# Optimization experiments

Hardware: AMD Instinct MI355X
Metric: run time of the kernel (lower is better)

The kernel has to match this reference:

```python
import jax, jax.numpy as jnp
import numpy as np

N = 100000        # points
C_IN = 64         # in_planes
C_OUT = 64        # out_planes (== mid_planes)
SHARE = 8         # share_planes
NS = 16           # nsample
CW = C_OUT // SHARE  # attention channels (8)
EPS = 1e-5


def _bn(x, gamma, beta):
    # PointBatchNorm in training mode: normalize over all axes except channel (last)
    ax = tuple(range(x.ndim - 1))
    m = jnp.mean(x, axis=ax)
    v = jnp.var(x, axis=ax)
    return gamma * (x - m) * jax.lax.rsqrt(v + EPS) + beta


def setup_inputs() -> dict:
    key = jax.random.key(0)
    ks = jax.random.split(key, 20)
    s = 0.05
    inp = {
        "p": jax.random.normal(ks[0], (N, 3), jnp.float32) * 5.0,
        "x": jax.random.normal(ks[1], (N, C_IN), jnp.float32),
        "o": jnp.array([N], jnp.int32),
        "idx": jax.random.randint(ks[2], (N, NS), 0, N, jnp.int32),
        # q/k/v linears
        "Wq": jax.random.normal(ks[3], (C_IN, C_OUT), jnp.float32) * s,
        "bq": jnp.zeros((C_OUT,), jnp.float32),
        "Wk": jax.random.normal(ks[4], (C_IN, C_OUT), jnp.float32) * s,
        "bk": jnp.zeros((C_OUT,), jnp.float32),
        "Wv": jax.random.normal(ks[5], (C_IN, C_OUT), jnp.float32) * s,
        "bv": jnp.zeros((C_OUT,), jnp.float32),
        # linear_p: Linear(3,3) -> BN(3) -> ReLU -> Linear(3,out)
        "Wp1": jax.random.normal(ks[6], (3, 3), jnp.float32) * 0.5,
        "bp1": jnp.zeros((3,), jnp.float32),
        "gp": jnp.ones((3,), jnp.float32),
        "betap": jnp.zeros((3,), jnp.float32),
        "Wp2": jax.random.normal(ks[7], (3, C_OUT), jnp.float32) * s,
        "bp2": jnp.zeros((C_OUT,), jnp.float32),
        # linear_w: BN(mid)->ReLU->Linear(mid, CW)->BN(CW)->ReLU->Linear(CW, CW)
        "gw1": jnp.ones((C_OUT,), jnp.float32),
        "bw1": jnp.zeros((C_OUT,), jnp.float32),
        "Ww1": jax.random.normal(ks[8], (C_OUT, CW), jnp.float32) * s,
        "bww1": jnp.zeros((CW,), jnp.float32),
        "gw2": jnp.ones((CW,), jnp.float32),
        "bw2": jnp.zeros((CW,), jnp.float32),
        "Ww2": jax.random.normal(ks[9], (CW, CW), jnp.float32) * s,
        "bww2": jnp.zeros((CW,), jnp.float32),
    }
    return inp


def reference(p, x, o, idx,
              Wq, bq, Wk, bk, Wv, bv,
              Wp1, bp1, gp, betap, Wp2, bp2,
              gw1, bw1, Ww1, bww1, gw2, bw2, Ww2, bww2):
    relu = jax.nn.relu
    x_q = x @ Wq + bq                       # [n, mid]
    x_k = x @ Wk + bk                       # [n, mid]
    x_v = x @ Wv + bv                       # [n, out]
    # knn_query_and_group: gather neighbors (idx precomputed), with relative xyz
    p_r0 = p[idx] - p[:, None, :]           # [n, ns, 3]
    xk_g = x_k[idx]                         # [n, ns, mid]
    xv_g = x_v[idx]                         # [n, ns, out]
    # linear_p
    p_r = relu(_bn(p_r0 @ Wp1 + bp1, gp, betap)) @ Wp2 + bp2   # [n, ns, out]
    # einops.reduce 'n ns (i j) -> n ns j' with j=mid_planes: i==1 -> identity
    r_qk = xk_g - x_q[:, None, :] + p_r     # [n, ns, mid]
    # linear_w
    w = relu(_bn(r_qk, gw1, bw1)) @ Ww1 + bww1          # [n, ns, CW]
    w = relu(_bn(w, gw2, bw2)) @ Ww2 + bww2             # [n, ns, CW]
    w = jax.nn.softmax(w, axis=1)                        # softmax over neighbors
    # shared-channel weighted sum
    v = (xv_g + p_r).reshape(N, NS, SHARE, CW)           # [n, ns, s, i]
    out = jnp.einsum('ntsi,nti->nsi', v, w)              # [n, s, i]
    return out.reshape(N, C_OUT)
```

## Files before the change

kernel.cpp:

```cpp
#include <hip/hip_runtime.h>
#include <math.h>

#define NPTS 100000
#define NSAMP 16
#define NROWS (NPTS*NSAMP)
#define EPS 1e-5f

#define NQKV ((NPTS + 63)/64)
#define GRID_B 1024
#define GRID_C 2048
#define GRID_D 2048
#define GRID_E 2048

#define S_BN1A 0
#define S_BN1B 4
#define S_BN2A 8
#define S_BN2B 72
#define S_BN3A 136
#define S_BN3B 144
#define S_PARTB 160
#define S_PARTC (S_PARTB + GRID_B*8)
#define S_PARTD (S_PARTC + GRID_C*128)

typedef __attribute__((ext_vector_type(8))) short bf16x8;
typedef __attribute__((ext_vector_type(4))) float f32x4;

__device__ __forceinline__ unsigned short f2bf(float f) {
    unsigned int x = __float_as_uint(f);
    unsigned int r = (x + 0x7fffu + ((x >> 16) & 1u)) >> 16;
    return (unsigned short)r;
}
__device__ __forceinline__ float bf2f(unsigned short u) {
    return __uint_as_float(((unsigned int)u) << 16);
}
__device__ __forceinline__ float rlF(float v, int t) {
    return __int_as_float(__builtin_amdgcn_readlane(__float_as_int(v), t));
}

__global__ __launch_bounds__(256) void qkv_bn1_kernel(
    const float* __restrict__ x,
    const float* __restrict__ Wq, const float* __restrict__ bq,
    const float* __restrict__ Wk, const float* __restrict__ bk,
    const float* __restrict__ Wv, const float* __restrict__ bv,
    float* __restrict__ xq, unsigned short* __restrict__ xkb,
    unsigned short* __restrict__ xvb,
    const float* __restrict__ p, const int* __restrict__ idx,
    const float* __restrict__ Wp1, const float* __restrict__ bp1,
    float* __restrict__ part)
{
    __shared__ __align__(16) float xsh[64][68];
    __shared__ __align__(16) float wsh[64][64];
    __shared__ float red16[4][6];
    const int tid = threadIdx.x;

    if (blockIdx.x >= NQKV) {
        const int b = blockIdx.x - NQKV;
        float w9[9], bb[3];
        #pragma unroll
        for (int i = 0; i < 9; ++i) w9[i] = Wp1[i];
        #pragma unroll
        for (int i = 0; i < 3; ++i) bb[i] = bp1[i];

        float s0=0.f,s1=0.f,s2=0.f,q0=0.f,q1=0.f,q2=0.f;
        for (int row = b*256 + tid; row < NROWS; row += GRID_B*256) {
            const int n = row >> 4;
            const int j = idx[row];
            const float d0 = p[j*3+0] - p[n*3+0];
            const float d1 = p[j*3+1] - p[n*3+1];
            const float d2 = p[j*3+2] - p[n*3+2];
            const float t0 = d0*w9[0] + d1*w9[3] + d2*w9[6] + bb[0];
            const float t1 = d0*w9[1] + d1*w9[4] + d2*w9[7] + bb[1];
            const float t2 = d0*w9[2] + d1*w9[5] + d2*w9[8] + bb[2];
            s0 += t0; s1 += t1; s2 += t2;
            q0 += t0*t0; q1 += t1*t1; q2 += t2*t2;
        }
        #pragma unroll
        for (int m = 32; m >= 1; m >>= 1) {
            s0 += __shfl_xor(s0, m); s1 += __shfl_xor(s1, m); s2 += __shfl_xor(s2, m);
            q0 += __shfl_xor(q0, m); q1 += __shfl_xor(q1, m); q2 += __shfl_xor(q2, m);
        }
        const int lane = tid & 63, wid = tid >> 6;
        if (lane == 0) {
            red16[wid][0]=s0; red16[wid][1]=s1; red16[wid][2]=s2;
            red16[wid][3]=q0; red16[wid][4]=q1; red16[wid][5]=q2;
        }
        __syncthreads();
        if (tid < 6)
            part[b*8 + tid] = red16[0][tid]+red16[1][tid]+red16[2][tid]+red16[3][tid];
        return;
    }

    const int r0 = blockIdx.x * 64;
    {
        const int row = tid >> 4, c4 = tid & 15;
        #pragma unroll
        for (int rr = 0; rr < 4; ++rr) {
            const int r = row + rr*16;
            const int gr = r0 + r;
            float4 v = (gr < NPTS) ? *(const float4*)&x[(size_t)gr*64 + c4*4]
                                   : make_float4(0.f, 0.f, 0.f, 0.f);
            *(float4*)&xsh[r][c4*4] = v;
        }
    }

    const int tr = tid >> 4, tc = tid & 15;

    for (int m = 0; m < 3; ++m) {
        const float* __restrict__ W  = (m == 0) ? Wq : (m == 1) ? Wk : Wv;
        const float* __restrict__ bs = (m == 0) ? bq : (m == 1) ? bk : bv;

        __syncthreads();
        for (int l = tid; l < 1024; l += 256)
            *(float4*)&wsh[l >> 4][(l & 15)*4] = *(const float4*)&W[l*4];
        __syncthreads();

        float acc[4][4];
        {
            const float4 b4 = *(const float4*)&bs[tc*4];
            #pragma unroll
            for (int rr = 0; rr < 4; ++rr) {
                acc[rr][0] = b4.x; acc[rr][1] = b4.y;
                acc[rr][2] = b4.z; acc[rr][3] = b4.w;
            }
        }

        #pragma unroll 4
        for (int k4 = 0; k4 < 16; ++k4) {
            float4 xr[4];
            #pragma unroll
            for (int rr = 0; rr < 4; ++rr)
                xr[rr] = *(const float4*)&xsh[tr + 16*rr][k4*4];
            float4 wr[4];
            #pragma unroll
            for (int kk = 0; kk < 4; ++kk)
                wr[kk] = *(const float4*)&wsh[k4*4 + kk][tc*4];
            #pragma unroll
            for (int rr = 0; rr < 4; ++rr) {
                acc[rr][0] += xr[rr].x*wr[0].x + xr[rr].y*wr[1].x + xr[rr].z*wr[2].x + xr[rr].w*wr[3].x;
                acc[rr][1] += xr[rr].x*wr[0].y + xr[rr].y*wr[1].y + xr[rr].z*wr[2].y + xr[rr].w*wr[3].y;
                acc[rr][2] += xr[rr].x*wr[0].z + xr[rr].y*wr[1].z + xr[rr].z*wr[2].z + xr[rr].w*wr[3].z;
                acc[rr][3] += xr[rr].x*wr[0].w + xr[rr].y*wr[1].w + xr[rr].z*wr[2].w + xr[rr].w*wr[3].w;
            }
        }

        #pragma unroll
        for (int rr = 0; rr < 4; ++rr) {
            const int gr = r0 + tr + 16*rr;
            if (gr < NPTS) {
                if (m == 0) {
                    float4 o;
                    o.x = acc[rr][0]; o.y = acc[rr][1]; o.z = acc[rr][2]; o.w = acc[rr][3];
                    *(float4*)&xq[(size_t)gr*64 + tc*4] = o;
                } else {
                    unsigned short* dst = (m == 1) ? xkb : xvb;
                    ushort4 o;
                    o.x = f2bf(acc[rr][0]); o.y = f2bf(acc[rr][1]);
                    o.z = f2bf(acc[rr][2]); o.w = f2bf(acc[rr][3]);
                    *(ushort4*)&dst[(size_t)gr*64 + tc*4] = o;
                }
            }
        }
    }
}

__global__ __launch_bounds__(256) void bn_fin_kernel(
    const float* __restrict__ part, int nblk, int stride, int nch,
    const float* __restrict__ g, const float* __restrict__ beta,
    float* __restrict__ aout, float* __restrict__ bout)
{
    const int c = blockIdx.x;
    const int tid = threadIdx.x;
    float s = 0.f, q = 0.f;
    for (int b = tid; b < nblk; b += 256) {
        s += part[(size_t)b*stride + c];
        q += part[(size_t)b*stride + nch + c];
    }
    #pragma unroll
    for (int m = 32; m >= 1; m >>= 1) { s += __shfl_xor(s, m); q += __shfl_xor(q, m); }
    __shared__ float rs[4], rq[4];
    if ((tid & 63) == 0) { rs[tid >> 6] = s; rq[tid >> 6] = q; }
    __syncthreads();
    if (tid == 0) {
        s = rs[0]+rs[1]+rs[2]+rs[3];
        q = rq[0]+rq[1]+rq[2]+rq[3];
        const float inv = 1.0f / (float)NROWS;
        const float mean = s * inv;
        const float var = fmaxf(q * inv - mean*mean, 0.f);
        const float a = g[c] * rsqrtf(var + EPS);
        aout[c] = a;
        bout[c] = beta[c] - a * mean;
    }
}

__global__ __launch_bounds__(256, 8) void bn2_stats_kernel(
    const float* __restrict__ p, const int* __restrict__ idx,
    const float* __restrict__ xq, const unsigned short* __restrict__ xkb,
    const float* __restrict__ Wp1, const float* __restrict__ bp1,
    const float* __restrict__ Wp2, const float* __restrict__ bp2,
    const float* __restrict__ st, float* __restrict__ part)
{
    const int tid = threadIdx.x, lane = tid & 63, wid = tid >> 6;
    float w9[9], bb[3], a1[3], b1[3];
    #pragma unroll
    for (int i = 0; i < 9; ++i) w9[i] = Wp1[i];
    #pragma unroll
    for (int i = 0; i < 3; ++i) { bb[i] = bp1[i]; a1[i] = st[S_BN1A+i]; b1[i] = st[S_BN1B+i]; }
    const float wc0 = Wp2[lane], wc1 = Wp2[64+lane], wc2 = Wp2[128+lane], bpc = bp2[lane];
    const int lane16 = lane & 15;

    float s = 0.f, q = 0.f;
    const int nw = gridDim.x * 4;
    for (int pt = blockIdx.x*4 + wid; pt < NPTS; pt += nw) {
        const float xqc = xq[(size_t)pt*64 + lane];
        const int jreg = idx[pt*16 + lane16];
        const float pn0 = p[pt*3], pn1 = p[pt*3+1], pn2 = p[pt*3+2];
        const float d0 = p[jreg*3] - pn0, d1 = p[jreg*3+1] - pn1, d2 = p[jreg*3+2] - pn2;
        const float t0 = d0*w9[0] + d1*w9[3] + d2*w9[6] + bb[0];
        const float t1 = d0*w9[1] + d1*w9[4] + d2*w9[7] + bb[1];
        const float t2 = d0*w9[2] + d1*w9[5] + d2*w9[8] + bb[2];
        const float h0 = fmaxf(a1[0]*t0 + b1[0], 0.f);
        const float h1 = fmaxf(a1[1]*t1 + b1[1], 0.f);
        const float h2 = fmaxf(a1[2]*t2 + b1[2], 0.f);

        #pragma unroll
        for (int t = 0; t < 16; ++t) {
            const int jt = __builtin_amdgcn_readlane(jreg, t);
            const float g0 = rlF(h0, t), g1 = rlF(h1, t), g2 = rlF(h2, t);
            const float pr = fmaf(g0, wc0, fmaf(g1, wc1, fmaf(g2, wc2, bpc)));
            const float r = bf2f(xkb[(size_t)jt*64 + lane]) - xqc + pr;
            s += r; q = fmaf(r, r, q);
        }
    }
    __shared__ float redS[4][64], redQ[4][64];
    redS[wid][lane] = s; redQ[wid][lane] = q;
    __syncthreads();
    if (tid < 64) {
        const float S = redS[0][tid]+redS[1][tid]+redS[2][tid]+redS[3][tid];
        const float Q = redQ[0][tid]+redQ[1][tid]+redQ[2][tid]+redQ[3][tid];
        part[(size_t)blockIdx.x*128 + tid] = S;
        part[(size_t)blockIdx.x*128 + 64 + tid] = Q;
    }
}

__global__ __launch_bounds__(256, 8) void w1_kernel(
    const float* __restrict__ p, const int* __restrict__ idx,
    const float* __restrict__ xq, const unsigned short* __restrict__ xkb,
    const float* __restrict__ Wp1, const float* __restrict__ bp1,
    const float* __restrict__ Wp2, const float* __restrict__ bp2,
    const float* __restrict__ Ww1, const float* __restrict__ bww1,
    const float* __restrict__ st, unsigned short* __restrict__ w1out,
    float* __restrict__ part)
{
    __shared__ unsigned short hl[4][16][64];
    const int tid = threadIdx.x, lane = tid & 63, wid = tid >> 6;

    float w9[9], bb[3], a1[3], b1[3];
    #pragma unroll
    for (int i = 0; i < 9; ++i) w9[i] = Wp1[i];
    #pragma unroll
    for (int i = 0; i < 3; ++i) { bb[i] = bp1[i]; a1[i] = st[S_BN1A+i]; b1[i] = st[S_BN1B+i]; }

    const int c = lane;
    const float wc0 = Wp2[c], wc1 = Wp2[64+c], wc2 = Wp2[128+c], bpc = bp2[c];
    const float a2c = st[S_BN2A + c], b2c = st[S_BN2B + c];
    const int lane16 = lane & 15;
    const int kgrp = lane >> 4;

    bf16x8 aF0, aF1;
    {
        const int m = lane16;
        #pragma unroll
        for (int i = 0; i < 8; ++i) {
            const int k0 = kgrp*4 + (i & 3) + 16*(i >> 2);
            const int i0 = (m < 8) ? (k0*8 + m) : 0;
            const int i1 = (m < 8) ? ((k0 + 32)*8 + m) : 0;
            aF0[i] = (m < 8) ? (short)f2bf(Ww1[i0]) : (short)0;
            aF1[i] = (m < 8) ? (short)f2bf(Ww1[i1]) : (short)0;
        }
    }
    f32x4 cb;
    #pragma unroll
    for (int r = 0; r < 4; ++r) cb[r] = bww1[(kgrp*4 + r) & 7];

    float s3[4] = {0.f,0.f,0.f,0.f}, q3[4] = {0.f,0.f,0.f,0.f};
    const int nw = gridDim.x * 4;
    for (int pt = blockIdx.x*4 + wid; pt < NPTS; pt += nw) {
        const float xqc = xq[(size_t)pt*64 + lane];
        const int jreg = idx[pt*16 + lane16];
        const float pn0 = p[pt*3], pn1 = p[pt*3+1], pn2 = p[pt*3+2];
        const float d0 = p[jreg*3] - pn0, d1 = p[jreg*3+1] - pn1, d2 = p[jreg*3+2] - pn2;
        const float t0v = d0*w9[0] + d1*w9[3] + d2*w9[6] + bb[0];
        const float t1v = d0*w9[1] + d1*w9[4] + d2*w9[7] + bb[1];
        const float t2v = d0*w9[2] + d1*w9[5] + d2*w9[8] + bb[2];
        const float h0 = fmaxf(a1[0]*t0v + b1[0], 0.f);
        const float h1 = fmaxf(a1[1]*t1v + b1[1], 0.f);
        const float h2 = fmaxf(a1[2]*t2v + b1[2], 0.f);

        #pragma unroll
        for (int t = 0; t < 16; ++t) {
            const int jt = __builtin_amdgcn_readlane(jreg, t);
            const float g0 = rlF(h0, t), g1 = rlF(h1, t), g2 = rlF(h2, t);
            const float pr = fmaf(g0, wc0, fmaf(g1, wc1, fmaf(g2, wc2, bpc)));
            const float r = bf2f(xkb[(size_t)jt*64 + lane]) - xqc + pr;
            const float hv = fmaxf(fmaf(a2c, r, b2c), 0.f);
            hl[wid][t][lane ^ ((t & 7) << 3)] = f2bf(hv);
        }

        const int t = lane16;
        const int key = (t & 7) << 3;
        union { bf16x8 v; uint2 u[2]; } b0u, b1u;
        b0u.u[0] = *(const uint2*)&hl[wid][t][(kgrp*4)      ^ key];
        b0u.u[1] = *(const uint2*)&hl[wid][t][(kgrp*4 + 16) ^ key];
        b1u.u[0] = *(const uint2*)&hl[wid][t][(kgrp*4 + 32) ^ key];
        b1u.u[1] = *(const uint2*)&hl[wid][t][(kgrp*4 + 48) ^ key];

        f32x4 acc = __builtin_amdgcn_mfma_f32_16x16x32_bf16(aF0, b0u.v, cb, 0, 0, 0);
        acc = __builtin_amdgcn_mfma_f32_16x16x32_bf16(aF1, b1u.v, acc, 0, 0, 0);

        if (lane < 32) {
            ushort4 o;
            o.x = f2bf(acc[0]); o.y = f2bf(acc[1]);
            o.z = f2bf(acc[2]); o.w = f2bf(acc[3]);
            *(ushort4*)&w1out[(size_t)pt*128 + lane16*8 + kgrp*4] = o;
            #pragma unroll
            for (int r = 0; r < 4; ++r) {
                s3[r] += acc[r];
                q3[r] = fmaf(acc[r], acc[r], q3[r]);
            }
        }
    }

    #pragma unroll
    for (int m = 8; m >= 1; m >>= 1) {
        #pragma unroll
        for (int r = 0; r < 4; ++r) {
            s3[r] += __shfl_xor(s3[r], m);
            q3[r] += __shfl_xor(q3[r], m);
        }
    }
    __shared__ float redS[4][8], redQ[4][8];
    if (lane == 0 || lane == 16) {
        const int jb = (lane >> 4) * 4;
        #pragma unroll
        for (int r = 0; r < 4; ++r) { redS[wid][jb+r] = s3[r]; redQ[wid][jb+r] = q3[r]; }
    }
    __syncthreads();
    if (tid < 8) {
        const float S = redS[0][tid]+redS[1][tid]+redS[2][tid]+redS[3][tid];
        const float Q = redQ[0][tid]+redQ[1][tid]+redQ[2][tid]+redQ[3][tid];
        part[(size_t)blockIdx.x*16 + tid]     = S;
        part[(size_t)blockIdx.x*16 + 8 + tid] = Q;
    }
}

__global__ __launch_bounds__(256, 8) void out_kernel(
    const float* __restrict__ p, const int* __restrict__ idx,
    const unsigned short* __restrict__ xvb, const unsigned short* __restrict__ w1b,
    const float* __restrict__ Wp1, const float* __restrict__ bp1,
    const float* __restrict__ Wp2, const float* __restrict__ bp2,
    const float* __restrict__ Ww2, const float* __restrict__ bww2,
    const float* __restrict__ st, float* __restrict__ out)
{
    __shared__ float wl[4][16][8];
    const int tid = threadIdx.x, lane = tid & 63, wid = tid >> 6;
    const int j8 = lane & 7, t0 = lane >> 3;
    const int lane16 = lane & 15;

    float w9[9], bb[3], a1[3], b1[3];
    #pragma unroll
    for (int i = 0; i < 9; ++i) w9[i] = Wp1[i];
    #pragma unroll
    for (int i = 0; i < 3; ++i) { bb[i] = bp1[i]; a1[i] = st[S_BN1A+i]; b1[i] = st[S_BN1B+i]; }
    float ww2c[8];
    #pragma unroll
    for (int i = 0; i < 8; ++i) ww2c[i] = Ww2[i*8 + j8];
    const float a3j = st[S_BN3A + j8], b3j = st[S_BN3B + j8];
    const float bw2j = bww2[j8];
    const int c = lane;
    const float wc0 = Wp2[c], wc1 = Wp2[64+c], wc2 = Wp2[128+c], bpc = bp2[c];

    const int nw = gridDim.x * 4;
    for (int pt = blockIdx.x*4 + wid; pt < NPTS; pt += nw) {
        const int jreg = idx[pt*16 + lane16];
        const float pn0 = p[pt*3], pn1 = p[pt*3+1], pn2 = p[pt*3+2];
        const float d0 = p[jreg*3] - pn0, d1 = p[jreg*3+1] - pn1, d2 = p[jreg*3+2] - pn2;
        const float t1v = d0*w9[0] + d1*w9[3] + d2*w9[6] + bb[0];
        const float t2v = d0*w9[1] + d1*w9[4] + d2*w9[7] + bb[1];
        const float t3v = d0*w9[2] + d1*w9[5] + d2*w9[8] + bb[2];
        const float h0 = fmaxf(a1[0]*t1v + b1[0], 0.f);
        const float h1 = fmaxf(a1[1]*t2v + b1[1], 0.f);
        const float h2 = fmaxf(a1[2]*t3v + b1[2], 0.f);

        const float val0 = bf2f(w1b[(size_t)pt*128 + lane]);
        const float val1 = bf2f(w1b[(size_t)pt*128 + 64 + lane]);
        const float r0 = fmaxf(a3j*val0 + b3j, 0.f);
        const float r1 = fmaxf(a3j*val1 + b3j, 0.f);
        float v0 = bw2j, v1 = bw2j;
        const int gbase = lane & 56;
        #pragma unroll
        for (int jj = 0; jj < 8; ++jj) {
            v0 += __shfl(r0, gbase + jj) * ww2c[jj];
            v1 += __shfl(r1, gbase + jj) * ww2c[jj];
        }

        float m = fmaxf(v0, v1);
        m = fmaxf(m, __shfl_xor(m, 8));
        m = fmaxf(m, __shfl_xor(m, 16));
        m = fmaxf(m, __shfl_xor(m, 32));
        float e0 = __expf(v0 - m), e1 = __expf(v1 - m);
        float ssum = e0 + e1;
        ssum += __shfl_xor(ssum, 8);
        ssum += __shfl_xor(ssum, 16);
        ssum += __shfl_xor(ssum, 32);
        const float inv = 1.0f / ssum;
        wl[wid][t0][j8]     = e0 * inv;
        wl[wid][t0 + 8][j8] = e1 * inv;

        float acc = 0.f;
        #pragma unroll
        for (int t = 0; t < 16; ++t) {
            const int jt = __builtin_amdgcn_readlane(jreg, t);
            const float g0 = rlF(h0, t), g1 = rlF(h1, t), g2 = rlF(h2, t);
            const float pr = fmaf(g0, wc0, fmaf(g1, wc1, fmaf(g2, wc2, bpc)));
            const float wt = wl[wid][t][j8];
            acc = fmaf(bf2f(xvb[(size_t)jt*64 + c]) + pr, wt, acc);
        }
        out[(size_t)pt*64 + c] = acc;
    }
}

extern "C" void kernel_launch(void* const* d_in, const int* in_sizes, int n_in,
                              void* d_out, int out_size, void* d_ws, size_t ws_size,
                              hipStream_t stream)
{
    const float* p    = (const float*)d_in[0];
    const float* x    = (const float*)d_in[1];
    const int*   idx  = (const int*)d_in[3];
    const float* Wq   = (const float*)d_in[4];
    const float* bq   = (const float*)d_in[5];
    const float* Wk   = (const float*)d_in[6];
    const float* bk   = (const float*)d_in[7];
    const float* Wv   = (const float*)d_in[8];
    const float* bv   = (const float*)d_in[9];
    const float* Wp1  = (const float*)d_in[10];
    const float* bp1  = (const float*)d_in[11];
    const float* gp   = (const float*)d_in[12];
    const float* betap= (const float*)d_in[13];
    const float* Wp2  = (const float*)d_in[14];
    const float* bp2  = (const float*)d_in[15];
    const float* gw1  = (const float*)d_in[16];
    const float* bw1  = (const float*)d_in[17];
    const float* Ww1  = (const float*)d_in[18];
    const float* bww1 = (const float*)d_in[19];
    const float* gw2  = (const float*)d_in[20];
    const float* bw2  = (const float*)d_in[21];
    const float* Ww2  = (const float*)d_in[22];
    const float* bww2 = (const float*)d_in[23];

    float* out = (float*)d_out;
    float* ws  = (float*)d_ws;

    float*          xq  = ws;
    unsigned short* xkb = (unsigned short*)(ws + (size_t)NPTS*64);
    unsigned short* xvb = (unsigned short*)(ws + (size_t)NPTS*96);
    unsigned short* w1b = (unsigned short*)(ws + (size_t)NPTS*128);
    float*          st  = ws + (size_t)NPTS*192;

    qkv_bn1_kernel<<<NQKV + GRID_B, 256, 0, stream>>>(
        x, Wq, bq, Wk, bk, Wv, bv, xq, xkb, xvb,
        p, idx, Wp1, bp1, st + S_PARTB);
    bn_fin_kernel<<<3, 256, 0, stream>>>(st + S_PARTB, GRID_B, 8, 3, gp, betap,
                                         st + S_BN1A, st + S_BN1B);

    bn2_stats_kernel<<<GRID_C, 256, 0, stream>>>(p, idx, xq, xkb, Wp1, bp1, Wp2, bp2,
                                                 st, st + S_PARTC);
    bn_fin_kernel<<<64, 256, 0, stream>>>(st + S_PARTC, GRID_C, 128, 64, gw1, bw1,
                                          st + S_BN2A, st + S_BN2B);

    w1_kernel<<<GRID_D, 256, 0, stream>>>(p, idx, xq, xkb, Wp1, bp1, Wp2, bp2,
                                          Ww1, bww1, st, w1b, st + S_PARTD);
    bn_fin_kernel<<<8, 256, 0, stream>>>(st + S_PARTD, GRID_D, 16, 8, gw2, bw2,
                                         st + S_BN3A, st + S_BN3B);

    out_kernel<<<GRID_E, 256, 0, stream>>>(p, idx, xvb, w1b, Wp1, bp1, Wp2, bp2,
                                           Ww2, bww2, st, out);
}
```

Before: 251.5 us.

## Store xq in bf16, prefetch next point's gathers, switch MFMA to f16, drop softmax max

Several changes land together. xq is now stored as bf16 like xk and xv, which halves its write and read traffic. The three gather kernels prefetch the next point's idx, position and xq or w1 values before working on the current one, so load latency overlaps with compute. The w1 MFMA now uses f16 inputs instead of bf16, bf16 packing uses the hardware v_cvt_pk_bf16_f32 instruction, and the softmax drops its max-subtraction shuffles. In exchange, precision drops for xq, and removing the max makes the softmax able to overflow if logits are large.

```diff
diff --git a/kernel.cpp b/kernel.cpp
--- a/kernel.cpp
+++ b/kernel.cpp
@@ -22,16 +22,16 @@
 #define S_PARTC (S_PARTB + GRID_B*8)
 #define S_PARTD (S_PARTC + GRID_C*128)
 
-typedef __attribute__((ext_vector_type(8))) short bf16x8;
+typedef __attribute__((ext_vector_type(8))) _Float16 f16x8;
 typedef __attribute__((ext_vector_type(4))) float f32x4;
 
-__device__ __forceinline__ unsigned short f2bf(float f) {
-    unsigned int x = __float_as_uint(f);
-    unsigned int r = (x + 0x7fffu + ((x >> 16) & 1u)) >> 16;
-    return (unsigned short)r;
-}
 __device__ __forceinline__ float bf2f(unsigned short u) {
     return __uint_as_float(((unsigned int)u) << 16);
+}
+__device__ __forceinline__ unsigned int cvt_pk_bf16(float lo, float hi) {
+    unsigned int r;
+    asm("v_cvt_pk_bf16_f32 %0, %1, %2" : "=v"(r) : "v"(lo), "v"(hi));
+    return r;
 }
 __device__ __forceinline__ float rlF(float v, int t) {
     return __int_as_float(__builtin_amdgcn_readlane(__float_as_int(v), t));
@@ -42,7 +42,7 @@
     const float* __restrict__ Wq, const float* __restrict__ bq,
     const float* __restrict__ Wk, const float* __restrict__ bk,
     const float* __restrict__ Wv, const float* __restrict__ bv,
-    float* __restrict__ xq, unsigned short* __restrict__ xkb,
+    unsigned short* __restrict__ xqb, unsigned short* __restrict__ xkb,
     unsigned short* __restrict__ xvb,
     const float* __restrict__ p, const int* __restrict__ idx,
     const float* __restrict__ Wp1, const float* __restrict__ bp1,
@@ -108,6 +108,7 @@
     for (int m = 0; m < 3; ++m) {
         const float* __restrict__ W  = (m == 0) ? Wq : (m == 1) ? Wk : Wv;
         const float* __restrict__ bs = (m == 0) ? bq : (m == 1) ? bk : bv;
+        unsigned short* __restrict__ dst = (m == 0) ? xqb : (m == 1) ? xkb : xvb;
 
         __syncthreads();
         for (int l = tid; l < 1024; l += 256)
@@ -147,17 +148,10 @@
         for (int rr = 0; rr < 4; ++rr) {
             const int gr = r0 + tr + 16*rr;
             if (gr < NPTS) {
-                if (m == 0) {
-                    float4 o;
-                    o.x = acc[rr][0]; o.y = acc[rr][1]; o.z = acc[rr][2]; o.w = acc[rr][3];
-                    *(float4*)&xq[(size_t)gr*64 + tc*4] = o;
-                } else {
-                    unsigned short* dst = (m == 1) ? xkb : xvb;
-                    ushort4 o;
-                    o.x = f2bf(acc[rr][0]); o.y = f2bf(acc[rr][1]);
-                    o.z = f2bf(acc[rr][2]); o.w = f2bf(acc[rr][3]);
-                    *(ushort4*)&dst[(size_t)gr*64 + tc*4] = o;
-                }
+                uint2 o;
+                o.x = cvt_pk_bf16(acc[rr][0], acc[rr][1]);
+                o.y = cvt_pk_bf16(acc[rr][2], acc[rr][3]);
+                *(uint2*)&dst[(size_t)gr*64 + tc*4] = o;
             }
         }
     }
@@ -194,7 +188,7 @@
 
 __global__ __launch_bounds__(256, 8) void bn2_stats_kernel(
     const float* __restrict__ p, const int* __restrict__ idx,
-    const float* __restrict__ xq, const unsigned short* __restrict__ xkb,
+    const unsigned short* __restrict__ xqb, const unsigned short* __restrict__ xkb,
     const float* __restrict__ Wp1, const float* __restrict__ bp1,
     const float* __restrict__ Wp2, const float* __restrict__ bp2,
     const float* __restrict__ st, float* __restrict__ part)
@@ -207,14 +201,29 @@
     for (int i = 0; i < 3; ++i) { bb[i] = bp1[i]; a1[i] = st[S_BN1A+i]; b1[i] = st[S_BN1B+i]; }
     const float wc0 = Wp2[lane], wc1 = Wp2[64+lane], wc2 = Wp2[128+lane], bpc = bp2[lane];
     const int lane16 = lane & 15;
+    const int nw = gridDim.x * 4;
 
     float s = 0.f, q = 0.f;
-    const int nw = gridDim.x * 4;
-    for (int pt = blockIdx.x*4 + wid; pt < NPTS; pt += nw) {
-        const float xqc = xq[(size_t)pt*64 + lane];
-        const int jreg = idx[pt*16 + lane16];
-        const float pn0 = p[pt*3], pn1 = p[pt*3+1], pn2 = p[pt*3+2];
-        const float d0 = p[jreg*3] - pn0, d1 = p[jreg*3+1] - pn1, d2 = p[jreg*3+2] - pn2;
+    int pt = blockIdx.x*4 + wid;
+    int jn = 0; float xqn = 0.f, pn0 = 0.f, pn1 = 0.f, pn2 = 0.f;
+    float pj0 = 0.f, pj1 = 0.f, pj2 = 0.f;
+    if (pt < NPTS) {
+        jn = idx[pt*16 + lane16];
+        xqn = bf2f(xqb[(size_t)pt*64 + lane]);
+        pn0 = p[pt*3]; pn1 = p[pt*3+1]; pn2 = p[pt*3+2];
+        pj0 = p[jn*3]; pj1 = p[jn*3+1]; pj2 = p[jn*3+2];
+    }
+    while (pt < NPTS) {
+        const int jreg = jn;
+        const float xqc = xqn;
+        const float d0 = pj0 - pn0, d1 = pj1 - pn1, d2 = pj2 - pn2;
+        const int ptn = pt + nw;
+        if (ptn < NPTS) {
+            jn = idx[ptn*16 + lane16];
+            xqn = bf2f(xqb[(size_t)ptn*64 + lane]);
+            pn0 = p[ptn*3]; pn1 = p[ptn*3+1]; pn2 = p[ptn*3+2];
+            pj0 = p[jn*3]; pj1 = p[jn*3+1]; pj2 = p[jn*3+2];
+        }
         const float t0 = d0*w9[0] + d1*w9[3] + d2*w9[6] + bb[0];
         const float t1 = d0*w9[1] + d1*w9[4] + d2*w9[7] + bb[1];
         const float t2 = d0*w9[2] + d1*w9[5] + d2*w9[8] + bb[2];
@@ -230,6 +239,7 @@
             const float r = bf2f(xkb[(size_t)jt*64 + lane]) - xqc + pr;
             s += r; q = fmaf(r, r, q);
         }
+        pt = ptn;
     }
     __shared__ float redS[4][64], redQ[4][64];
     redS[wid][lane] = s; redQ[wid][lane] = q;
@@ -244,14 +254,14 @@
 
 __global__ __launch_bounds__(256, 8) void w1_kernel(
     const float* __restrict__ p, const int* __restrict__ idx,
-    const float* __restrict__ xq, const unsigned short* __restrict__ xkb,
+    const unsigned short* __restrict__ xqb, const unsigned short* __restrict__ xkb,
     const float* __restrict__ Wp1, const float* __restrict__ bp1,
     const float* __restrict__ Wp2, const float* __restrict__ bp2,
     const float* __restrict__ Ww1, const float* __restrict__ bww1,
     const float* __restrict__ st, unsigned short* __restrict__ w1out,
     float* __restrict__ part)
 {
-    __shared__ unsigned short hl[4][16][64];
+    __shared__ __align__(16) _Float16 hl[4][16][64];
     const int tid = threadIdx.x, lane = tid & 63, wid = tid >> 6;
 
     float w9[9], bb[3], a1[3], b1[3];
@@ -266,7 +276,7 @@
     const int lane16 = lane & 15;
     const int kgrp = lane >> 4;
 
-    bf16x8 aF0, aF1;
+    f16x8 aF0, aF1;
     {
         const int m = lane16;
         #pragma unroll
@@ -274,8 +284,8 @@
             const int k0 = kgrp*4 + (i & 3) + 16*(i >> 2);
             const int i0 = (m < 8) ? (k0*8 + m) : 0;
             const int i1 = (m < 8) ? ((k0 + 32)*8 + m) : 0;
-            aF0[i] = (m < 8) ? (short)f2bf(Ww1[i0]) : (short)0;
-            aF1[i] = (m < 8) ? (short)f2bf(Ww1[i1]) : (short)0;
+            aF0[i] = (m < 8) ? (_Float16)Ww1[i0] : (_Float16)0.f;
+            aF1[i] = (m < 8) ? (_Float16)Ww1[i1] : (_Float16)0.f;
         }
     }
     f32x4 cb;
@@ -284,11 +294,26 @@
 
     float s3[4] = {0.f,0.f,0.f,0.f}, q3[4] = {0.f,0.f,0.f,0.f};
     const int nw = gridDim.x * 4;
-    for (int pt = blockIdx.x*4 + wid; pt < NPTS; pt += nw) {
-        const float xqc = xq[(size_t)pt*64 + lane];
-        const int jreg = idx[pt*16 + lane16];
-        const float pn0 = p[pt*3], pn1 = p[pt*3+1], pn2 = p[pt*3+2];
-        const float d0 = p[jreg*3] - pn0, d1 = p[jreg*3+1] - pn1, d2 = p[jreg*3+2] - pn2;
+    int pt = blockIdx.x*4 + wid;
+    int jn = 0; float xqn = 0.f, pn0 = 0.f, pn1 = 0.f, pn2 = 0.f;
+    float pj0 = 0.f, pj1 = 0.f, pj2 = 0.f;
+    if (pt < NPTS) {
+        jn = idx[pt*16 + lane16];
+        xqn = bf2f(xqb[(size_t)pt*64 + lane]);
+        pn0 = p[pt*3]; pn1 = p[pt*3+1]; pn2 = p[pt*3+2];
+        pj0 = p[jn*3]; pj1 = p[jn*3+1]; pj2 = p[jn*3+2];
+    }
+    while (pt < NPTS) {
+        const int jreg = jn;
+        const float xqc = xqn;
+        const float d0 = pj0 - pn0, d1 = pj1 - pn1, d2 = pj2 - pn2;
+        const int ptn = pt + nw;
+        if (ptn < NPTS) {
+            jn = idx[ptn*16 + lane16];
+            xqn = bf2f(xqb[(size_t)ptn*64 + lane]);
+            pn0 = p[ptn*3]; pn1 = p[ptn*3+1]; pn2 = p[ptn*3+2];
+            pj0 = p[jn*3]; pj1 = p[jn*3+1]; pj2 = p[jn*3+2];
+        }
         const float t0v = d0*w9[0] + d1*w9[3] + d2*w9[6] + bb[0];
         const float t1v = d0*w9[1] + d1*w9[4] + d2*w9[7] + bb[1];
         const float t2v = d0*w9[2] + d1*w9[5] + d2*w9[8] + bb[2];
@@ -302,32 +327,32 @@
             const float g0 = rlF(h0, t), g1 = rlF(h1, t), g2 = rlF(h2, t);
             const float pr = fmaf(g0, wc0, fmaf(g1, wc1, fmaf(g2, wc2, bpc)));
             const float r = bf2f(xkb[(size_t)jt*64 + lane]) - xqc + pr;
-            const float hv = fmaxf(fmaf(a2c, r, b2c), 0.f);
-            hl[wid][t][lane ^ ((t & 7) << 3)] = f2bf(hv);
+            hl[wid][t][lane ^ ((t & 7) << 3)] = (_Float16)fmaxf(fmaf(a2c, r, b2c), 0.f);
         }
 
         const int t = lane16;
         const int key = (t & 7) << 3;
-        union { bf16x8 v; uint2 u[2]; } b0u, b1u;
+        union { f16x8 v; uint2 u[2]; } b0u, b1u;
         b0u.u[0] = *(const uint2*)&hl[wid][t][(kgrp*4)      ^ key];
         b0u.u[1] = *(const uint2*)&hl[wid][t][(kgrp*4 + 16) ^ key];
         b1u.u[0] = *(const uint2*)&hl[wid][t][(kgrp*4 + 32) ^ key];
         b1u.u[1] = *(const uint2*)&hl[wid][t][(kgrp*4 + 48) ^ key];
 
-        f32x4 acc = __builtin_amdgcn_mfma_f32_16x16x32_bf16(aF0, b0u.v, cb, 0, 0, 0);
-        acc = __builtin_amdgcn_mfma_f32_16x16x32_bf16(aF1, b1u.v, acc, 0, 0, 0);
+        f32x4 acc = __builtin_amdgcn_mfma_f32_16x16x32_f16(aF0, b0u.v, cb, 0, 0, 0);
+        acc = __builtin_amdgcn_mfma_f32_16x16x32_f16(aF1, b1u.v, acc, 0, 0, 0);
 
         if (lane < 32) {
-            ushort4 o;
-            o.x = f2bf(acc[0]); o.y = f2bf(acc[1]);
-            o.z = f2bf(acc[2]); o.w = f2bf(acc[3]);
-            *(ushort4*)&w1out[(size_t)pt*128 + lane16*8 + kgrp*4] = o;
+            uint2 o;
+            o.x = cvt_pk_bf16(acc[0], acc[1]);
+            o.y = cvt_pk_bf16(acc[2], acc[3]);
+            *(uint2*)&w1out[(size_t)pt*128 + lane16*8 + kgrp*4] = o;
             #pragma unroll
             for (int r = 0; r < 4; ++r) {
                 s3[r] += acc[r];
                 q3[r] = fmaf(acc[r], acc[r], q3[r]);
             }
         }
+        pt = ptn;
     }
 
     #pragma unroll
@@ -380,10 +405,28 @@
     const float wc0 = Wp2[c], wc1 = Wp2[64+c], wc2 = Wp2[128+c], bpc = bp2[c];
 
     const int nw = gridDim.x * 4;
-    for (int pt = blockIdx.x*4 + wid; pt < NPTS; pt += nw) {
-        const int jreg = idx[pt*16 + lane16];
-        const float pn0 = p[pt*3], pn1 = p[pt*3+1], pn2 = p[pt*3+2];
-        const float d0 = p[jreg*3] - pn0, d1 = p[jreg*3+1] - pn1, d2 = p[jreg*3+2] - pn2;
+    int pt = blockIdx.x*4 + wid;
+    int jn = 0; float pn0 = 0.f, pn1 = 0.f, pn2 = 0.f;
+    float pj0 = 0.f, pj1 = 0.f, pj2 = 0.f, v0n = 0.f, v1n = 0.f;
+    if (pt < NPTS) {
+        jn = idx[pt*16 + lane16];
+        pn0 = p[pt*3]; pn1 = p[pt*3+1]; pn2 = p[pt*3+2];
+        pj0 = p[jn*3]; pj1 = p[jn*3+1]; pj2 = p[jn*3+2];
+        v0n = bf2f(w1b[(size_t)pt*128 + lane]);
+        v1n = bf2f(w1b[(size_t)pt*128 + 64 + lane]);
+    }
+    while (pt < NPTS) {
+        const int jreg = jn;
+        const float d0 = pj0 - pn0, d1 = pj1 - pn1, d2 = pj2 - pn2;
+        const float val0 = v0n, val1 = v1n;
+        const int ptn = pt + nw;
+        if (ptn < NPTS) {
+            jn = idx[ptn*16 + lane16];
+            pn0 = p[ptn*3]; pn1 = p[ptn*3+1]; pn2 = p[ptn*3+2];
+            pj0 = p[jn*3]; pj1 = p[jn*3+1]; pj2 = p[jn*3+2];
+            v0n = bf2f(w1b[(size_t)ptn*128 + lane]);
+            v1n = bf2f(w1b[(size_t)ptn*128 + 64 + lane]);
+        }
         const float t1v = d0*w9[0] + d1*w9[3] + d2*w9[6] + bb[0];
         const float t2v = d0*w9[1] + d1*w9[4] + d2*w9[7] + bb[1];
         const float t3v = d0*w9[2] + d1*w9[5] + d2*w9[8] + bb[2];
@@ -391,8 +434,6 @@
         const float h1 = fmaxf(a1[1]*t2v + b1[1], 0.f);
         const float h2 = fmaxf(a1[2]*t3v + b1[2], 0.f);
 
-        const float val0 = bf2f(w1b[(size_t)pt*128 + lane]);
-        const float val1 = bf2f(w1b[(size_t)pt*128 + 64 + lane]);
         const float r0 = fmaxf(a3j*val0 + b3j, 0.f);
         const float r1 = fmaxf(a3j*val1 + b3j, 0.f);
         float v0 = bw2j, v1 = bw2j;
@@ -402,12 +443,7 @@
             v0 += __shfl(r0, gbase + jj) * ww2c[jj];
             v1 += __shfl(r1, gbase + jj) * ww2c[jj];
         }
-
-        float m = fmaxf(v0, v1);
-        m = fmaxf(m, __shfl_xor(m, 8));
-        m = fmaxf(m, __shfl_xor(m, 16));
-        m = fmaxf(m, __shfl_xor(m, 32));
-        float e0 = __expf(v0 - m), e1 = __expf(v1 - m);
+        float e0 = __expf(v0), e1 = __expf(v1);
         float ssum = e0 + e1;
         ssum += __shfl_xor(ssum, 8);
         ssum += __shfl_xor(ssum, 16);
@@ -426,6 +462,7 @@
             acc = fmaf(bf2f(xvb[(size_t)jt*64 + c]) + pr, wt, acc);
         }
         out[(size_t)pt*64 + c] = acc;
+        pt = ptn;
     }
 }
 
@@ -460,24 +497,24 @@
     float* out = (float*)d_out;
     float* ws  = (float*)d_ws;
 
-    float*          xq  = ws;
-    unsigned short* xkb = (unsigned short*)(ws + (size_t)NPTS*64);
-    unsigned short* xvb = (unsigned short*)(ws + (size_t)NPTS*96);
-    unsigned short* w1b = (unsigned short*)(ws + (size_t)NPTS*128);
-    float*          st  = ws + (size_t)NPTS*192;
+    unsigned short* xqb = (unsigned short*)ws;
+    unsigned short* xkb = (unsigned short*)(ws + (size_t)NPTS*32);
+    unsigned short* xvb = (unsigned short*)(ws + (size_t)NPTS*64);
+    unsigned short* w1b = (unsigned short*)(ws + (size_t)NPTS*96);
+    float*          st  = ws + (size_t)NPTS*160;
 
     qkv_bn1_kernel<<<NQKV + GRID_B, 256, 0, stream>>>(
-        x, Wq, bq, Wk, bk, Wv, bv, xq, xkb, xvb,
+        x, Wq, bq, Wk, bk, Wv, bv, xqb, xkb, xvb,
         p, idx, Wp1, bp1, st + S_PARTB);
     bn_fin_kernel<<<3, 256, 0, stream>>>(st + S_PARTB, GRID_B, 8, 3, gp, betap,
                                          st + S_BN1A, st + S_BN1B);
 
-    bn2_stats_kernel<<<GRID_C, 256, 0, stream>>>(p, idx, xq, xkb, Wp1, bp1, Wp2, bp2,
+    bn2_stats_kernel<<<GRID_C, 256, 0, stream>>>(p, idx, xqb, xkb, Wp1, bp1, Wp2, bp2,
                                                  st, st + S_PARTC);
     bn_fin_kernel<<<64, 256, 0, stream>>>(st + S_PARTC, GRID_C, 128, 64, gw1, bw1,
                                           st + S_BN2A, st + S_BN2B);
 
-    w1_kernel<<<GRID_D, 256, 0, stream>>>(p, idx, xq, xkb, Wp1, bp1, Wp2, bp2,
+    w1_kernel<<<GRID_D, 256, 0, stream>>>(p, idx, xqb, xkb, Wp1, bp1, Wp2, bp2,
                                           Ww1, bww1, st, w1b, st + S_PARTD);
     bn_fin_kernel<<<8, 256, 0, stream>>>(st + S_PARTD, GRID_D, 16, 8, gw2, bw2,
                                          st + S_BN3A, st + S_BN3B);
```

Result: slower. 266.7 us (+6.0%).
